# Kernel optimization log

Measured on AMD Instinct MI355X. Metric: run time of the kernel, lower is better.

Reference implementation:

```python
import jax, jax.numpy as jnp
import numpy as np
import math

B = 512
EMB = 512
CLASSNUM = 70722
M = 0.4
H = 0.333
S = 64.0
EPS = 1e-3


def setup_inputs() -> dict:
    key = jax.random.key(0)
    k1, k2, k3, k4, k5 = jax.random.split(key, 5)
    embbedings = jax.random.normal(k1, (B, EMB), dtype=jnp.float32)
    # feature norms: positive, realistic range ~[1, 30)
    norms = jax.random.uniform(k2, (B, 1), dtype=jnp.float32) * 29.0 + 1.0
    label = jax.random.randint(k3, (B,), 0, CLASSNUM, dtype=jnp.int64)
    class_sample_num_ = jax.random.uniform(k4, (B,), dtype=jnp.float32) * 9.0 + 1.0
    kernel = jax.random.normal(k5, (EMB, CLASSNUM), dtype=jnp.float32)
    return {
        "embbedings": embbedings,
        "norms": norms,
        "label": label,
        "class_sample_num_": class_sample_num_,
        "kernel": kernel,
    }


def reference(embbedings, norms, label, class_sample_num_, kernel):
    # l2-normalize kernel columns (axis=0)
    kernel_norm = kernel / jnp.linalg.norm(kernel, axis=0, keepdims=True)
    cosine = jnp.matmul(embbedings, kernel_norm)  # [B, C]
    cosine = jnp.clip(cosine, -1.0 + EPS, 1.0 - EPS)

    # detached margin scaler path (torch uses .detach / no_grad)
    safe_norms = jnp.clip(norms, 0.001, 100.0)
    safe_norms = safe_norms / (class_sample_num_[:, None] + 0.001)
    safe_norms = jnp.clip(safe_norms, 0.001, 100.0)
    safe_norms = jax.lax.stop_gradient(safe_norms)

    mean = jnp.mean(safe_norms)
    std = jnp.std(safe_norms, ddof=1)  # torch.std is unbiased
    # t_alpha = 1.0 => batch stats are exactly this batch's mean/std
    batch_mean, batch_std = mean, std

    margin_scaler = (safe_norms - batch_mean) / (batch_std + EPS)
    margin_scaler = jnp.clip(margin_scaler * H, -1.0, 1.0)  # [B, 1]
    ms = margin_scaler[:, 0]  # [B]

    rows = jnp.arange(B)
    lab = label.astype(jnp.int32)

    # angular margin: theta_m = clip(theta + onehot * (-m*ms))
    theta = jnp.arccos(cosine)
    theta = theta.at[rows, lab].add(-M * ms)
    theta_m = jnp.clip(theta, EPS, math.pi - EPS)
    cosine2 = jnp.cos(theta_m)

    # additive margin at the label column: g_add = m + m*ms
    cosine2 = cosine2.at[rows, lab].add(-(M + M * ms))

    return cosine2 * S
```

## Files before the change

kernel.cpp:

```cpp
#include <hip/hip_runtime.h>
#include <hip/hip_bf16.h>
#include <math.h>

#define CLASSNUM 70722
#define BATCH 512
#define EMBD 512
#define M_C 0.4f
#define H_C 0.333f
#define S_C 64.0f
#define EPS_C 0.001f
#define PI_F 3.14159265358979f

typedef __bf16 bf16_t;
typedef __bf16 bf16x8 __attribute__((ext_vector_type(8)));
typedef float f32x4 __attribute__((ext_vector_type(4)));

__device__ __forceinline__ float clampf(float x, float lo, float hi) {
    return fminf(fmaxf(x, lo), hi);
}

__global__ __launch_bounds__(256) void prep_kernel(
    const float* __restrict__ emb, const float* __restrict__ norms,
    const float* __restrict__ csn, bf16_t* __restrict__ Aws,
    float* __restrict__ msw)
{
    __shared__ float sred[256];
    const int tid = threadIdx.x;
    if (blockIdx.x == 0) {
        float s0, s1;
        {
            float sn = clampf(norms[tid], 0.001f, 100.0f);
            sn = sn / (csn[tid] + 0.001f);
            s0 = clampf(sn, 0.001f, 100.0f);
        }
        {
            float sn = clampf(norms[tid + 256], 0.001f, 100.0f);
            sn = sn / (csn[tid + 256] + 0.001f);
            s1 = clampf(sn, 0.001f, 100.0f);
        }
        sred[tid] = s0 + s1;
        __syncthreads();
        for (int off = 128; off > 0; off >>= 1) {
            if (tid < off) sred[tid] += sred[tid + off];
            __syncthreads();
        }
        const float mean = sred[0] * (1.0f / 512.0f);
        __syncthreads();
        const float d0 = s0 - mean, d1 = s1 - mean;
        sred[tid] = d0 * d0 + d1 * d1;
        __syncthreads();
        for (int off = 128; off > 0; off >>= 1) {
            if (tid < off) sred[tid] += sred[tid + off];
            __syncthreads();
        }
        const float stdv = sqrtf(sred[0] * (1.0f / 511.0f));
        const float inv = 1.0f / (stdv + EPS_C);
        msw[tid]       = clampf(d0 * inv * H_C, -1.0f, 1.0f);
        msw[tid + 256] = clampf(d1 * inv * H_C, -1.0f, 1.0f);
    } else {
        const int base = ((blockIdx.x - 1) * 256 + tid) * 4;
        const float4 v = *(const float4*)(emb + base);
        bf16_t h[4] = {(bf16_t)v.x, (bf16_t)v.y, (bf16_t)v.z, (bf16_t)v.w};
        *(unsigned long long*)(Aws + base) = *(unsigned long long*)h;
    }
}

__global__ __launch_bounds__(64) void lab_kernel(
    const float* __restrict__ emb, const int* __restrict__ label,
    const float* __restrict__ kmat, const float* __restrict__ msw,
    float* __restrict__ labout)
{
    const int b = blockIdx.x;
    const int l = threadIdx.x;
    const int lab = label[b];
    const float* col = kmat + lab;
    const float* e = emb + b * EMBD;
    float dot = 0.0f, ss = 0.0f;
    for (int k = l; k < EMBD; k += 64) {
        const float kv = col[(size_t)k * CLASSNUM];
        const float ev = e[k];
        dot = fmaf(ev, kv, dot);
        ss  = fmaf(kv, kv, ss);
    }
    for (int off = 32; off > 0; off >>= 1) {
        dot += __shfl_down(dot, off);
        ss  += __shfl_down(ss, off);
    }
    if (l == 0) {
        float c = dot / sqrtf(ss);
        c = clampf(c, -1.0f + EPS_C, 1.0f - EPS_C);
        const float msv = msw[b];
        float th = acosf(c) - M_C * msv;
        th = clampf(th, EPS_C, PI_F - EPS_C);
        labout[b] = (cosf(th) - (M_C + M_C * msv)) * S_C;
    }
}

__global__ __launch_bounds__(256) void gemm_kernel(
    const bf16_t* __restrict__ Aws, const float* __restrict__ Kmat,
    float* __restrict__ out)
{
    __shared__ bf16_t Alds[128 * 40];
    __shared__ bf16_t Blds[128 * 40];
    __shared__ float red[256];
    __shared__ float invn[128];

    const int bid = blockIdx.x;
    const int n0 = (bid >> 2) << 7;
    const int m0 = (bid & 3) << 7;
    const int tid = threadIdx.x;
    const int lane = tid & 63;
    const int wave = tid >> 6;
    const int quad = lane >> 4;
    const int r16  = lane & 15;
    const int wm = (wave >> 1) * 64;
    const int wn = (wave & 1) * 64;

    const int n_loc = tid & 127;
    const int which = tid >> 7;
    const int n_g = n0 + n_loc;
    const bool nvalid = (n_g < CLASSNUM);
    const float* bptr = Kmat + n_g;

    const int am0 = tid >> 2, as0 = tid & 3;
    const int am1 = am0 + 64;
    const bf16_t* aptr0 = Aws + (size_t)(m0 + am0) * EMBD + as0 * 8;
    const bf16_t* aptr1 = Aws + (size_t)(m0 + am1) * EMBD + as0 * 8;
    bf16_t* const awr0 = &Alds[am0 * 40 + as0 * 8];
    bf16_t* const awr1 = &Alds[am1 * 40 + as0 * 8];
    bf16_t* const bwr0 = &Blds[n_loc * 40 + which * 8];
    bf16_t* const bwr1 = &Blds[n_loc * 40 + which * 8 + 16];

    f32x4 acc[4][4];
    const f32x4 zero = {0.0f, 0.0f, 0.0f, 0.0f};
#pragma unroll
    for (int i = 0; i < 4; ++i)
#pragma unroll
        for (int j = 0; j < 4; ++j) acc[i][j] = zero;

    float ssq = 0.0f;

    for (int it = 0; it < 16; ++it) {
        const int k0 = it * 32;
        const bf16x8 av0 = *(const bf16x8*)(aptr0 + k0);
        const bf16x8 av1 = *(const bf16x8*)(aptr1 + k0);
        float bv[16];
#pragma unroll
        for (int h = 0; h < 2; ++h) {
            const int kb = k0 + which * 8 + h * 16;
#pragma unroll
            for (int j = 0; j < 8; ++j)
                bv[h * 8 + j] = nvalid ? bptr[(size_t)(kb + j) * CLASSNUM] : 0.0f;
        }
        *(bf16x8*)awr0 = av0;
        *(bf16x8*)awr1 = av1;
#pragma unroll
        for (int h = 0; h < 2; ++h) {
            bf16x8 bw;
#pragma unroll
            for (int j = 0; j < 8; ++j) {
                const float v = bv[h * 8 + j];
                ssq = fmaf(v, v, ssq);
                bw[j] = (bf16_t)v;
            }
            *(bf16x8*)(h ? bwr1 : bwr0) = bw;
        }
        __syncthreads();

        bf16x8 afr[4], bfr[4];
#pragma unroll
        for (int mi = 0; mi < 4; ++mi)
            afr[mi] = *(const bf16x8*)(&Alds[(wm + mi * 16 + r16) * 40 + quad * 8]);
#pragma unroll
        for (int ni = 0; ni < 4; ++ni)
            bfr[ni] = *(const bf16x8*)(&Blds[(wn + ni * 16 + r16) * 40 + quad * 8]);
#pragma unroll
        for (int mi = 0; mi < 4; ++mi)
#pragma unroll
            for (int ni = 0; ni < 4; ++ni)
                acc[mi][ni] = __builtin_amdgcn_mfma_f32_16x16x32_bf16(
                    afr[mi], bfr[ni], acc[mi][ni], 0, 0, 0);
        __syncthreads();
    }

    red[tid] = ssq;
    __syncthreads();
    if (tid < 128) {
        const float s = red[tid] + red[tid + 128];
        invn[tid] = (s > 0.0f) ? (1.0f / sqrtf(s)) : 0.0f;
    }
    __syncthreads();

#pragma unroll
    for (int ni = 0; ni < 4; ++ni) {
        const int col_loc = wn + ni * 16 + r16;
        const int col = n0 + col_loc;
        if (col < CLASSNUM) {
            const float inv = invn[col_loc];
#pragma unroll
            for (int mi = 0; mi < 4; ++mi) {
                const int row = m0 + wm + mi * 16 + quad * 4;
                const f32x4 a = acc[mi][ni];
#pragma unroll
                for (int rr = 0; rr < 4; ++rr) {
                    const float c = clampf(a[rr] * inv, -1.0f + EPS_C, 1.0f - EPS_C);
                    out[(size_t)(row + rr) * CLASSNUM + col] = c * S_C;
                }
            }
        }
    }
}

__global__ __launch_bounds__(512) void scatter_kernel(
    const int* __restrict__ label, const float* __restrict__ labout,
    float* __restrict__ out)
{
    const int t = threadIdx.x;
    out[(size_t)t * CLASSNUM + label[t]] = labout[t];
}

extern "C" void kernel_launch(void* const* d_in, const int* in_sizes, int n_in,
                              void* d_out, int out_size, void* d_ws, size_t ws_size,
                              hipStream_t stream)
{
    const float* emb   = (const float*)d_in[0];
    const float* norms = (const float*)d_in[1];
    const int*   label = (const int*)d_in[2];
    const float* csn   = (const float*)d_in[3];
    const float* kmat  = (const float*)d_in[4];
    float* out = (float*)d_out;

    const size_t A_BYTES = (size_t)BATCH * EMBD * sizeof(bf16_t);
    if (ws_size < A_BYTES + 4096) return;
    bf16_t* Aws   = (bf16_t*)d_ws;
    float* msw    = (float*)((char*)d_ws + A_BYTES);
    float* labout = (float*)((char*)d_ws + A_BYTES + 2048);

    prep_kernel<<<257, 256, 0, stream>>>(emb, norms, csn, Aws, msw);
    lab_kernel<<<BATCH, 64, 0, stream>>>(emb, label, kmat, msw, labout);
    const int ntiles = (CLASSNUM + 127) / 128;
    gemm_kernel<<<ntiles * 4, 256, 0, stream>>>(Aws, kmat, out);
    scatter_kernel<<<1, 512, 0, stream>>>(label, labout, out);
}
```

Baseline: 374.6 us.

## Retile GEMM to full-batch 512x64 tiles with double-buffered async A loads

Each block now computes all 512 batch rows for 64 classes, so every kernel column is read from global memory and converted once instead of four times. The embedding is pre-laid out in k-tile-major bf16 form so whole A k-slices can be copied straight into LDS with global_load_lds. A and B are double-buffered, so the next tile's loads overlap the current MFMAs, and a single barrier per iteration replaces two. The cost is more accumulators per thread (128 floats), about 72KB of LDS per block, and an occupancy hint of 2.

```diff
diff --git a/kernel.cpp b/kernel.cpp
--- a/kernel.cpp
+++ b/kernel.cpp
@@ -19,6 +19,12 @@
     return fminf(fmaxf(x, lo), hi);
 }
 
+__device__ __forceinline__ void async_copy16(const bf16_t* g, bf16_t* l) {
+    __builtin_amdgcn_global_load_lds(
+        (const __attribute__((address_space(1))) unsigned int*)g,
+        (__attribute__((address_space(3))) unsigned int*)l, 16, 0, 0);
+}
+
 __global__ __launch_bounds__(256) void prep_kernel(
     const float* __restrict__ emb, const float* __restrict__ norms,
     const float* __restrict__ csn, bf16_t* __restrict__ Aws,
@@ -58,10 +64,14 @@
         msw[tid]       = clampf(d0 * inv * H_C, -1.0f, 1.0f);
         msw[tid + 256] = clampf(d1 * inv * H_C, -1.0f, 1.0f);
     } else {
-        const int base = ((blockIdx.x - 1) * 256 + tid) * 4;
-        const float4 v = *(const float4*)(emb + base);
+        const int f = ((blockIdx.x - 1) * 256 + tid) * 4;
+        const int m = f >> 9;
+        const int k = f & 511;
+        const int kt = k >> 5, ko = k & 31;
+        const float4 v = *(const float4*)(emb + f);
         bf16_t h[4] = {(bf16_t)v.x, (bf16_t)v.y, (bf16_t)v.z, (bf16_t)v.w};
-        *(unsigned long long*)(Aws + base) = *(unsigned long long*)h;
+        *(unsigned long long*)(Aws + kt * (512 * 32) + m * 32 + ko) =
+            *(unsigned long long*)h;
     }
 }
 
@@ -96,110 +106,114 @@
     }
 }
 
-__global__ __launch_bounds__(256) void gemm_kernel(
+__global__ __launch_bounds__(256, 2) void gemm_kernel(
     const bf16_t* __restrict__ Aws, const float* __restrict__ Kmat,
     float* __restrict__ out)
 {
-    __shared__ bf16_t Alds[128 * 40];
-    __shared__ bf16_t Blds[128 * 40];
+    __shared__ bf16_t Alds[2][512 * 32];
+    __shared__ bf16_t Blds[2][64 * 32];
     __shared__ float red[256];
-    __shared__ float invn[128];
-
-    const int bid = blockIdx.x;
-    const int n0 = (bid >> 2) << 7;
-    const int m0 = (bid & 3) << 7;
-    const int tid = threadIdx.x;
+    __shared__ float invn[64];
+
+    const int tid  = threadIdx.x;
     const int lane = tid & 63;
     const int wave = tid >> 6;
     const int quad = lane >> 4;
     const int r16  = lane & 15;
-    const int wm = (wave >> 1) * 64;
-    const int wn = (wave & 1) * 64;
-
-    const int n_loc = tid & 127;
-    const int which = tid >> 7;
-    const int n_g = n0 + n_loc;
-    const bool nvalid = (n_g < CLASSNUM);
-    const float* bptr = Kmat + n_g;
-
-    const int am0 = tid >> 2, as0 = tid & 3;
-    const int am1 = am0 + 64;
-    const bf16_t* aptr0 = Aws + (size_t)(m0 + am0) * EMBD + as0 * 8;
-    const bf16_t* aptr1 = Aws + (size_t)(m0 + am1) * EMBD + as0 * 8;
-    bf16_t* const awr0 = &Alds[am0 * 40 + as0 * 8];
-    bf16_t* const awr1 = &Alds[am1 * 40 + as0 * 8];
-    bf16_t* const bwr0 = &Blds[n_loc * 40 + which * 8];
-    bf16_t* const bwr1 = &Blds[n_loc * 40 + which * 8 + 16];
-
-    f32x4 acc[4][4];
+    const int n0   = blockIdx.x * 64;
+
+    const int bc = tid & 63;
+    const int bh = tid >> 6;
+    const bool nv = (n0 + bc) < CLASSNUM;
+    const float* bp = Kmat + (size_t)(n0 + bc);
+
+    f32x4 acc[8][4];
     const f32x4 zero = {0.0f, 0.0f, 0.0f, 0.0f};
 #pragma unroll
-    for (int i = 0; i < 4; ++i)
+    for (int i = 0; i < 8; ++i)
 #pragma unroll
         for (int j = 0; j < 4; ++j) acc[i][j] = zero;
 
     float ssq = 0.0f;
+    float bv[8];
+
+#pragma unroll
+    for (int j = 0; j < 8; ++j)
+        bv[j] = nv ? bp[(size_t)(bh * 8 + j) * CLASSNUM] : 0.0f;
+#pragma unroll
+    for (int i = 0; i < 8; ++i)
+        async_copy16(Aws + i * 2048 + wave * 512 + lane * 8,
+                     &Alds[0][i * 2048 + wave * 512]);
+    {
+        bf16x8 bw;
+#pragma unroll
+        for (int j = 0; j < 8; ++j) {
+            const float v = bv[j];
+            ssq = fmaf(v, v, ssq);
+            bw[j] = (bf16_t)v;
+        }
+        *(bf16x8*)&Blds[0][bc * 32 + bh * 8] = bw;
+    }
 
     for (int it = 0; it < 16; ++it) {
-        const int k0 = it * 32;
-        const bf16x8 av0 = *(const bf16x8*)(aptr0 + k0);
-        const bf16x8 av1 = *(const bf16x8*)(aptr1 + k0);
-        float bv[16];
-#pragma unroll
-        for (int h = 0; h < 2; ++h) {
-            const int kb = k0 + which * 8 + h * 16;
+        const int buf = it & 1;
+        __syncthreads();
+
+        if (it < 15) {
+            const size_t kb = (size_t)((it + 1) * 32 + bh * 8) * CLASSNUM;
 #pragma unroll
             for (int j = 0; j < 8; ++j)
-                bv[h * 8 + j] = nvalid ? bptr[(size_t)(kb + j) * CLASSNUM] : 0.0f;
-        }
-        *(bf16x8*)awr0 = av0;
-        *(bf16x8*)awr1 = av1;
-#pragma unroll
-        for (int h = 0; h < 2; ++h) {
+                bv[j] = nv ? bp[kb + (size_t)j * CLASSNUM] : 0.0f;
+            const bf16_t* gs = Aws + (size_t)(it + 1) * 16384;
+#pragma unroll
+            for (int i = 0; i < 8; ++i)
+                async_copy16(gs + i * 2048 + wave * 512 + lane * 8,
+                             &Alds[buf ^ 1][i * 2048 + wave * 512]);
+        }
+
+        bf16x8 bfr[4];
+#pragma unroll
+        for (int ni = 0; ni < 4; ++ni)
+            bfr[ni] = *(const bf16x8*)&Blds[buf][(ni * 16 + r16) * 32 + quad * 8];
+#pragma unroll
+        for (int mi = 0; mi < 8; ++mi) {
+            const bf16x8 af = *(const bf16x8*)
+                &Alds[buf][(wave * 128 + mi * 16 + r16) * 32 + quad * 8];
+#pragma unroll
+            for (int ni = 0; ni < 4; ++ni)
+                acc[mi][ni] = __builtin_amdgcn_mfma_f32_16x16x32_bf16(
+                    af, bfr[ni], acc[mi][ni], 0, 0, 0);
+        }
+
+        if (it < 15) {
             bf16x8 bw;
 #pragma unroll
             for (int j = 0; j < 8; ++j) {
-                const float v = bv[h * 8 + j];
+                const float v = bv[j];
                 ssq = fmaf(v, v, ssq);
                 bw[j] = (bf16_t)v;
             }
-            *(bf16x8*)(h ? bwr1 : bwr0) = bw;
-        }
-        __syncthreads();
-
-        bf16x8 afr[4], bfr[4];
-#pragma unroll
-        for (int mi = 0; mi < 4; ++mi)
-            afr[mi] = *(const bf16x8*)(&Alds[(wm + mi * 16 + r16) * 40 + quad * 8]);
-#pragma unroll
-        for (int ni = 0; ni < 4; ++ni)
-            bfr[ni] = *(const bf16x8*)(&Blds[(wn + ni * 16 + r16) * 40 + quad * 8]);
-#pragma unroll
-        for (int mi = 0; mi < 4; ++mi)
-#pragma unroll
-            for (int ni = 0; ni < 4; ++ni)
-                acc[mi][ni] = __builtin_amdgcn_mfma_f32_16x16x32_bf16(
-                    afr[mi], bfr[ni], acc[mi][ni], 0, 0, 0);
-        __syncthreads();
+            *(bf16x8*)&Blds[buf ^ 1][bc * 32 + bh * 8] = bw;
+        }
     }
 
     red[tid] = ssq;
     __syncthreads();
-    if (tid < 128) {
-        const float s = red[tid] + red[tid + 128];
+    if (tid < 64) {
+        const float s = red[tid] + red[tid + 64] + red[tid + 128] + red[tid + 192];
         invn[tid] = (s > 0.0f) ? (1.0f / sqrtf(s)) : 0.0f;
     }
     __syncthreads();
 
 #pragma unroll
     for (int ni = 0; ni < 4; ++ni) {
-        const int col_loc = wn + ni * 16 + r16;
+        const int col_loc = ni * 16 + r16;
         const int col = n0 + col_loc;
         if (col < CLASSNUM) {
             const float inv = invn[col_loc];
 #pragma unroll
-            for (int mi = 0; mi < 4; ++mi) {
-                const int row = m0 + wm + mi * 16 + quad * 4;
+            for (int mi = 0; mi < 8; ++mi) {
+                const int row = wave * 128 + mi * 16 + quad * 4;
                 const f32x4 a = acc[mi][ni];
 #pragma unroll
                 for (int rr = 0; rr < 4; ++rr) {
@@ -238,7 +252,7 @@
 
     prep_kernel<<<257, 256, 0, stream>>>(emb, norms, csn, Aws, msw);
     lab_kernel<<<BATCH, 64, 0, stream>>>(emb, label, kmat, msw, labout);
-    const int ntiles = (CLASSNUM + 127) / 128;
-    gemm_kernel<<<ntiles * 4, 256, 0, stream>>>(Aws, kmat, out);
+    const int nblk = (CLASSNUM + 63) / 64;
+    gemm_kernel<<<nblk, 256, 0, stream>>>(Aws, kmat, out);
     scatter_kernel<<<1, 512, 0, stream>>>(label, labout, out);
 }
```

Result: slower. 401.3 us (+7.1%).
